# Optimization experiments

Measured on AMD Instinct MI355X. Metric: run time of the kernel, lower is better.

The kernel has to match this reference:

```python
import jax, jax.numpy as jnp
import numpy as np

B, D, H = 4096, 1024, 1024

def _glorot(key, shape):
    fan_in, fan_out = shape
    limit = np.sqrt(6.0 / (fan_in + fan_out))
    return jax.random.uniform(key, shape, jnp.float32, -limit, limit)

def setup_inputs() -> dict:
    key = jax.random.key(0)
    ks = jax.random.split(key, 12)
    inp = {
        'inputs': jax.random.normal(ks[0], (B, D), jnp.float32),
        'h_prev': jax.random.normal(ks[1], (B, H), jnp.float32),
        'c_prev': jax.random.normal(ks[2], (B, H), jnp.float32),
    }
    names = ['f', 'i', 'c', 'o']
    for j, n in enumerate(names):
        inp['W_' + n] = _glorot(ks[3 + 2 * j], (D, H))
        inp['U_' + n] = _glorot(ks[4 + 2 * j], (H, H))
        inp['b_' + n] = jnp.zeros((H,), jnp.float32)
    return inp

def reference(inputs, h_prev, c_prev, W_f, U_f, b_f, W_i, U_i, b_i, W_c, U_c, b_c, W_o, U_o, b_o):
    f_t = jax.nn.sigmoid(inputs @ W_f + h_prev @ U_f + b_f)
    i_t = jax.nn.sigmoid(inputs @ W_i + h_prev @ U_i + b_i)
    c_tilde = jnp.tanh(inputs @ W_c + h_prev @ U_c + b_c)
    c_next = f_t * c_prev + i_t * c_tilde
    o_t = jax.nn.sigmoid(inputs @ W_o + h_prev @ U_o + b_o)
    h_next = o_t * jnp.tanh(c_next)
    return (h_next, c_next)
```

## Files before the change

kernel.cpp:

```cpp
#include <hip/hip_runtime.h>


typedef __attribute__((ext_vector_type(8))) short bfrag8;

__device__ __forceinline__ unsigned int f2bf(float f) {
  unsigned int u = __builtin_bit_cast(unsigned int, f);
  unsigned int r = (u + 0x7fffu + ((u >> 16) & 1u)) >> 16;
  return r & 0xffffu;
}

__global__ __launch_bounds__(256) void prep_x(const float* __restrict__ inputs,
                                              const float* __restrict__ h_prev,
                                              unsigned short* __restrict__ X) {
  int idx = blockIdx.x * 256 + threadIdx.x;
  int b  = idx >> 8;
  int k8 = (idx & 255) * 8;
  const float* src = (k8 < 1024) ? (inputs + (size_t)b * 1024 + k8)
                                 : (h_prev + (size_t)b * 1024 + (k8 - 1024));
  float4 v0 = ((const float4*)src)[0];
  float4 v1 = ((const float4*)src)[1];
  uint4 o;
  o.x = f2bf(v0.x) | (f2bf(v0.y) << 16);
  o.y = f2bf(v0.z) | (f2bf(v0.w) << 16);
  o.z = f2bf(v1.x) | (f2bf(v1.y) << 16);
  o.w = f2bf(v1.z) | (f2bf(v1.w) << 16);
  *(uint4*)(X + (size_t)b * 2048 + k8) = o;
}

__global__ __launch_bounds__(256) void prep_w(
    const float* __restrict__ s0, const float* __restrict__ s1,
    const float* __restrict__ s2, const float* __restrict__ s3,
    const float* __restrict__ s4, const float* __restrict__ s5,
    const float* __restrict__ s6, const float* __restrict__ s7,
    unsigned short* __restrict__ Wct) {
  int blk = blockIdx.x;
  int m = blk >> 8;
  const float* src = (m == 0) ? s0 : (m == 1) ? s1 : (m == 2) ? s2 : (m == 3) ? s3
                   : (m == 4) ? s4 : (m == 5) ? s5 : (m == 6) ? s6 : s7;
  int g = m >> 1, half = m & 1;
  unsigned short* dst = Wct + (size_t)g * 1024 * 2048 + (size_t)half * 1024;
  int t = blk & 255;
  int k0 = (t >> 4) * 64;
  int h0 = (t & 15) * 64;
  __shared__ float lt[64][68];
  int tid = threadIdx.x;
  #pragma unroll
  for (int it = 0; it < 4; ++it) {
    int r  = (tid >> 4) + it * 16;
    int c4 = (tid & 15) * 4;
    float4 v = *(const float4*)(src + (size_t)(k0 + r) * 1024 + h0 + c4);
    lt[r][c4 + 0] = v.x; lt[r][c4 + 1] = v.y; lt[r][c4 + 2] = v.z; lt[r][c4 + 3] = v.w;
  }
  __syncthreads();
  #pragma unroll
  for (int it = 0; it < 4; ++it) {
    int hh  = (tid >> 4) + it * 16;
    int kk4 = (tid & 15) * 4;
    uint2 o;
    o.x = f2bf(lt[kk4 + 0][hh]) | (f2bf(lt[kk4 + 1][hh]) << 16);
    o.y = f2bf(lt[kk4 + 2][hh]) | (f2bf(lt[kk4 + 3][hh]) << 16);
    *(uint2*)(dst + (size_t)(h0 + hh) * 2048 + k0 + kk4) = o;
  }
}


#define FENCE() asm volatile("" ::: "memory")
#define BARRIER() do { FENCE(); __builtin_amdgcn_s_barrier(); FENCE(); } while (0)
#define VMCNT(n) asm volatile("s_waitcnt vmcnt(" #n ")" ::: "memory")
#define LGKM(n) asm volatile("s_waitcnt lgkmcnt(" #n ")" ::: "memory")
#define GLOAD16(gp, lp) __builtin_amdgcn_global_load_lds( \
    (const __attribute__((address_space(1))) unsigned int*)(gp), \
    (__attribute__((address_space(3))) unsigned int*)(lp), 16, 0, 0)
#define DSR(dst, addr, off) asm volatile("ds_read_b128 %0, %1 offset:%c2" \
    : "=v"(dst) : "v"(addr), "n"(off))

#define AC "a0","a1","a2","a3","a4","a5","a6","a7","a8","a9","a10","a11","a12","a13","a14","a15", \
 "a16","a17","a18","a19","a20","a21","a22","a23","a24","a25","a26","a27","a28","a29","a30","a31", \
 "a32","a33","a34","a35","a36","a37","a38","a39","a40","a41","a42","a43","a44","a45","a46","a47", \
 "a48","a49","a50","a51","a52","a53","a54","a55","a56","a57","a58","a59","a60","a61","a62","a63", \
 "a64","a65","a66","a67","a68","a69","a70","a71","a72","a73","a74","a75","a76","a77","a78","a79", \
 "a80","a81","a82","a83","a84","a85","a86","a87","a88","a89","a90","a91","a92","a93","a94","a95", \
 "a96","a97","a98","a99","a100","a101","a102","a103","a104","a105","a106","a107","a108","a109","a110","a111", \
 "a112","a113","a114","a115","a116","a117","a118","a119","a120","a121","a122","a123","a124","a125","a126","a127"

#define WZ(n) "v_accvgpr_write_b32 a" #n ", 0\n\t"
#define AINIT() asm volatile( \
 WZ(0)WZ(1)WZ(2)WZ(3)WZ(4)WZ(5)WZ(6)WZ(7)WZ(8)WZ(9)WZ(10)WZ(11)WZ(12)WZ(13)WZ(14)WZ(15) \
 WZ(16)WZ(17)WZ(18)WZ(19)WZ(20)WZ(21)WZ(22)WZ(23)WZ(24)WZ(25)WZ(26)WZ(27)WZ(28)WZ(29)WZ(30)WZ(31) \
 WZ(32)WZ(33)WZ(34)WZ(35)WZ(36)WZ(37)WZ(38)WZ(39)WZ(40)WZ(41)WZ(42)WZ(43)WZ(44)WZ(45)WZ(46)WZ(47) \
 WZ(48)WZ(49)WZ(50)WZ(51)WZ(52)WZ(53)WZ(54)WZ(55)WZ(56)WZ(57)WZ(58)WZ(59)WZ(60)WZ(61)WZ(62)WZ(63) \
 WZ(64)WZ(65)WZ(66)WZ(67)WZ(68)WZ(69)WZ(70)WZ(71)WZ(72)WZ(73)WZ(74)WZ(75)WZ(76)WZ(77)WZ(78)WZ(79) \
 WZ(80)WZ(81)WZ(82)WZ(83)WZ(84)WZ(85)WZ(86)WZ(87)WZ(88)WZ(89)WZ(90)WZ(91)WZ(92)WZ(93)WZ(94)WZ(95) \
 WZ(96)WZ(97)WZ(98)WZ(99)WZ(100)WZ(101)WZ(102)WZ(103)WZ(104)WZ(105)WZ(106)WZ(107)WZ(108)WZ(109)WZ(110)WZ(111) \
 WZ(112)WZ(113)WZ(114)WZ(115)WZ(116)WZ(117)WZ(118)WZ(119)WZ(120)WZ(121)WZ(122)WZ(123)WZ(124)WZ(125)WZ(126)WZ(127) \
 ::: AC)

#define MFMA_ONE(BR, AF, BF) asm volatile( \
    "v_mfma_f32_16x16x32_bf16 a[" BR "], %0, %1, a[" BR "]" \
    :: "v"(AF), "v"(BF) : AC)

#define CLUSTER16(A4, B4, R00,R01,R02,R03, R10,R11,R12,R13, R20,R21,R22,R23, R30,R31,R32,R33) do { \
  __builtin_amdgcn_s_setprio(1); \
  MFMA_ONE(R00, (A4)[0], (B4)[0]); MFMA_ONE(R01, (A4)[1], (B4)[0]); \
  MFMA_ONE(R02, (A4)[2], (B4)[0]); MFMA_ONE(R03, (A4)[3], (B4)[0]); \
  MFMA_ONE(R10, (A4)[0], (B4)[1]); MFMA_ONE(R11, (A4)[1], (B4)[1]); \
  MFMA_ONE(R12, (A4)[2], (B4)[1]); MFMA_ONE(R13, (A4)[3], (B4)[1]); \
  MFMA_ONE(R20, (A4)[0], (B4)[2]); MFMA_ONE(R21, (A4)[1], (B4)[2]); \
  MFMA_ONE(R22, (A4)[2], (B4)[2]); MFMA_ONE(R23, (A4)[3], (B4)[2]); \
  MFMA_ONE(R30, (A4)[0], (B4)[3]); MFMA_ONE(R31, (A4)[1], (B4)[3]); \
  MFMA_ONE(R32, (A4)[2], (B4)[3]); MFMA_ONE(R33, (A4)[3], (B4)[3]); \
  __builtin_amdgcn_s_setprio(0); \
} while (0)

#define CL_MH0(A4, B4) CLUSTER16(A4, B4, \
  "0:3","4:7","8:11","12:15", "32:35","36:39","40:43","44:47", \
  "64:67","68:71","72:75","76:79", "96:99","100:103","104:107","108:111")
#define CL_MH1(A4, B4) CLUSTER16(A4, B4, \
  "16:19","20:23","24:27","28:31", "48:51","52:55","56:59","60:63", \
  "80:83","84:87","88:91","92:95", "112:115","116:119","120:123","124:127")

#define READ_A4(arr, BUF, MH, ABASE) do { \
  DSR(arr[0], ABASE, (BUF)*32768 + (MH)*8192 + 0);    \
  DSR(arr[1], ABASE, (BUF)*32768 + (MH)*8192 + 2048); \
  DSR(arr[2], ABASE, (BUF)*32768 + (MH)*8192 + 4096); \
  DSR(arr[3], ABASE, (BUF)*32768 + (MH)*8192 + 6144); \
} while (0)

#define READ_B4N(arr, BUF, BBASE) do { \
  DSR(arr[0], BBASE, (BUF)*32768 + 0);    \
  DSR(arr[1], BBASE, (BUF)*32768 + 2048); \
  DSR(arr[2], BBASE, (BUF)*32768 + 4096); \
  DSR(arr[3], BBASE, (BUF)*32768 + 6144); \
} while (0)

#define STAGE_A(BUF, H, kt) do { int _kb = ((kt) < 32 ? (kt) : 31) * 64; \
  GLOAD16(pA0 + (size_t)(H) * 262144 + _kb, smem + (BUF)*32768 + (H)*16384 + stbase); \
  GLOAD16(pA1 + (size_t)(H) * 262144 + _kb, smem + (BUF)*32768 + (H)*16384 + stbase + 1024); \
} while (0)

#define STAGE_B(BUF, kt) do { int _kb = ((kt) < 32 ? (kt) : 31) * 64; \
  GLOAD16(pB00 + _kb, smem + 65536 + (BUF)*32768 + stbase); \
  GLOAD16(pB01 + _kb, smem + 65536 + (BUF)*32768 + stbase + 1024); \
  GLOAD16(pB10 + _kb, smem + 65536 + (BUF)*32768 + 16384 + stbase); \
  GLOAD16(pB11 + _kb, smem + 65536 + (BUF)*32768 + 16384 + stbase + 1024); \
} while (0)

#define ARD(X, RS) asm volatile("v_accvgpr_read_b32 %0, " RS : "=v"(X))

#define EPI_M(Mi, F0,F1,F2,F3, I0,I1,I2,I3, C0,C1,C2,C3, O0,O1,O2,O3) do { \
  float pf[4], pi[4], pc[4], po[4]; \
  ARD(pf[0],F0); ARD(pf[1],F1); ARD(pf[2],F2); ARD(pf[3],F3); \
  ARD(pi[0],I0); ARD(pi[1],I1); ARD(pi[2],I2); ARD(pi[3],I3); \
  ARD(pc[0],C0); ARD(pc[1],C1); ARD(pc[2],C2); ARD(pc[3],C3); \
  ARD(po[0],O0); ARD(po[1],O1); ARD(po[2],O2); ARD(po[3],O3); \
  _Pragma("unroll") for (int j = 0; j < 4; ++j) { \
    const int b = rbw + (Mi) * 16 + q * 4 + j; \
    float xf = pf[j] + Bgf, xi = pi[j] + Bgi, xc = pc[j] + Bgc, xo = po[j] + Bgo; \
    float fg = 1.f / (1.f + __expf(-xf)); \
    float ig = 1.f / (1.f + __expf(-xi)); \
    float ct = 2.f / (1.f + __expf(-2.f * xc)) - 1.f; \
    float og = 1.f / (1.f + __expf(-xo)); \
    float cn = fg * c_prev[(size_t)b * 1024 + hcol] + ig * ct; \
    float hn = og * (2.f / (1.f + __expf(-2.f * cn)) - 1.f); \
    out[(size_t)b * 1024 + hcol] = hn; \
    out[(size_t)4194304 + (size_t)b * 1024 + hcol] = cn; \
  } \
} while (0)

__global__ __launch_bounds__(512, 2) void lstm_gemm(
    const unsigned short* __restrict__ X, const unsigned short* __restrict__ Wct,
    const float* __restrict__ c_prev,
    const float* __restrict__ bfv, const float* __restrict__ biv,
    const float* __restrict__ bcv, const float* __restrict__ bov,
    float* __restrict__ out) {
  extern __shared__ __align__(16) char smem[];
  const int tid = threadIdx.x;
  const int lane = tid & 63, w = tid >> 6;
  const int u = lane & 15, q = (lane >> 4) & 3;
  const int wm = w >> 2, wn = w & 3;

  const int bid = blockIdx.x;
  const int swz = (bid & 7) * 32 + (bid >> 3);
  const int h0 = (swz & 15) * 64;
  const int row0 = (swz >> 4) * 256;

  const unsigned lds0 = (unsigned)(size_t)((__attribute__((address_space(3))) char*)smem);

  const int sw0 = (q ^ (u & 7)) << 4;
  const int sw1 = ((q + 4) ^ (u & 7)) << 4;
  const unsigned aA0 = lds0 + wm * 16384 + u * 128 + sw0;
  const unsigned aA1 = lds0 + wm * 16384 + u * 128 + sw1;
  const unsigned aB0 = lds0 + 65536 + (wn * 64 + u) * 128 + sw0;
  const unsigned aB1 = lds0 + 65536 + (wn * 64 + u) * 128 + sw1;

  const int stbase = w * 2048 + lane * 16;
  const int rA0 = w * 16 + (lane >> 3), rA1 = rA0 + 8;
  const int ssA = (lane & 7) ^ (rA0 & 7);
  const unsigned short* pA0 = X + (size_t)(row0 + rA0) * 2048 + ssA * 8;
  const unsigned short* pA1 = X + (size_t)(row0 + rA1) * 2048 + ssA * 8;
  auto wrow = [&](int C) { return (((C >> 4) & 3) << 10) + h0 + ((C >> 6) << 4) + (C & 15); };
  const unsigned short* pB00 = Wct + (size_t)wrow(rA0) * 2048 + ssA * 8;
  const unsigned short* pB01 = Wct + (size_t)wrow(rA1) * 2048 + ssA * 8;
  const unsigned short* pB10 = Wct + (size_t)wrow(128 + rA0) * 2048 + ssA * 8;
  const unsigned short* pB11 = Wct + (size_t)wrow(128 + rA1) * 2048 + ssA * 8;

  AINIT();

  bfrag8 Ab0[4], Ab1[4], Bb0[4], Bb1[4];

  STAGE_A(0, 0, 0); STAGE_A(0, 1, 0);
  STAGE_B(0, 0);
  STAGE_B(1, 1);
  VMCNT(4);
  BARRIER();
  READ_A4(Ab0, 0, 0, aA0);
  READ_B4N(Bb0, 0, aB0);

  #pragma unroll 1
  for (int t = 0; t < 16; ++t) {
    const int kt1 = 2 * t + 1, kt2 = 2 * t + 2, kt3 = 2 * t + 3;
    READ_A4(Ab1, 0, 1, aA0);
    STAGE_A(1, 0, kt1); STAGE_A(1, 1, kt1);
    BARRIER(); LGKM(4);
    CL_MH0(Ab0, Bb0);
    READ_A4(Ab0, 0, 0, aA1);
    READ_B4N(Bb1, 0, aB1);
    BARRIER(); LGKM(8);
    CL_MH1(Ab1, Bb0);
    READ_A4(Ab1, 0, 1, aA1);
    VMCNT(0);
    BARRIER(); LGKM(4);
    CL_MH0(Ab0, Bb1);
    READ_A4(Ab0, 1, 0, aA0);
    READ_B4N(Bb0, 1, aB0);
    STAGE_B(0, kt2);
    BARRIER(); LGKM(8);
    CL_MH1(Ab1, Bb1);
    READ_A4(Ab1, 1, 1, aA0);
    STAGE_A(0, 0, kt2); STAGE_A(0, 1, kt2);
    BARRIER(); LGKM(4);
    CL_MH0(Ab0, Bb0);
    READ_A4(Ab0, 1, 0, aA1);
    READ_B4N(Bb1, 1, aB1);
    BARRIER(); LGKM(8);
    CL_MH1(Ab1, Bb0);
    READ_A4(Ab1, 1, 1, aA1);
    VMCNT(0);
    BARRIER(); LGKM(4);
    CL_MH0(Ab0, Bb1);
    READ_A4(Ab0, 0, 0, aA0);
    READ_B4N(Bb0, 0, aB0);
    STAGE_B(1, kt3);
    BARRIER(); LGKM(8);
    CL_MH1(Ab1, Bb1);
  }
  VMCNT(0); LGKM(0);
  asm volatile("s_nop 7\n\ts_nop 7");

  const int hcol = h0 + wn * 16 + u;
  const float Bgf = bfv[hcol], Bgi = biv[hcol], Bgc = bcv[hcol], Bgo = bov[hcol];
  const int rbw = row0 + wm * 128;
  EPI_M(0, "a0","a1","a2","a3",     "a32","a33","a34","a35",
           "a64","a65","a66","a67", "a96","a97","a98","a99");
  EPI_M(1, "a4","a5","a6","a7",     "a36","a37","a38","a39",
           "a68","a69","a70","a71", "a100","a101","a102","a103");
  EPI_M(2, "a8","a9","a10","a11",   "a40","a41","a42","a43",
           "a72","a73","a74","a75", "a104","a105","a106","a107");
  EPI_M(3, "a12","a13","a14","a15", "a44","a45","a46","a47",
           "a76","a77","a78","a79", "a108","a109","a110","a111");
  EPI_M(4, "a16","a17","a18","a19", "a48","a49","a50","a51",
           "a80","a81","a82","a83", "a112","a113","a114","a115");
  EPI_M(5, "a20","a21","a22","a23", "a52","a53","a54","a55",
           "a84","a85","a86","a87", "a116","a117","a118","a119");
  EPI_M(6, "a24","a25","a26","a27", "a56","a57","a58","a59",
           "a88","a89","a90","a91", "a120","a121","a122","a123");
  EPI_M(7, "a28","a29","a30","a31", "a60","a61","a62","a63",
           "a92","a93","a94","a95", "a124","a125","a126","a127");
}

extern "C" void kernel_launch(void* const* d_in, const int* in_sizes, int n_in,
                              void* d_out, int out_size, void* d_ws, size_t ws_size,
                              hipStream_t stream) {
  const float* inputs = (const float*)d_in[0];
  const float* h_prev = (const float*)d_in[1];
  const float* c_prev = (const float*)d_in[2];
  const float* Wf = (const float*)d_in[3];
  const float* Uf = (const float*)d_in[4];
  const float* bf = (const float*)d_in[5];
  const float* Wi = (const float*)d_in[6];
  const float* Ui = (const float*)d_in[7];
  const float* bi = (const float*)d_in[8];
  const float* Wc = (const float*)d_in[9];
  const float* Uc = (const float*)d_in[10];
  const float* bc = (const float*)d_in[11];
  const float* Wo = (const float*)d_in[12];
  const float* Uo = (const float*)d_in[13];
  const float* bo = (const float*)d_in[14];
  float* out = (float*)d_out;

  unsigned short* X   = (unsigned short*)d_ws;
  unsigned short* Wct = X + (size_t)4096 * 2048;

  (void)hipFuncSetAttribute(reinterpret_cast<const void*>(lstm_gemm),
                            hipFuncAttributeMaxDynamicSharedMemorySize, 131072);

  prep_x<<<4096, 256, 0, stream>>>(inputs, h_prev, X);
  prep_w<<<2048, 256, 0, stream>>>(Wf, Uf, Wi, Ui, Wc, Uc, Wo, Uo, Wct);
  lstm_gemm<<<256, 512, 131072, stream>>>(X, Wct, c_prev, bf, bi, bc, bo, out);
}
```

Before: 87.58 us.

## Shrink GEMM tile to 256x128 with K=32 steps for higher occupancy

The GEMM block tile drops from 256 rows by 256 gate-columns to 256 rows by 128 columns, with K-steps of 32 instead of 64. Each wave now holds 64 accumulators instead of 128, LDS use falls from 128 KiB to 48 KiB, and launch bounds ask for four blocks per CU. The intricate half-tile interleaved software pipeline is replaced by a simple double-buffered loop that waits on all loads and barriers twice per iteration. The aim is more blocks (512) and better occupancy to fill all CUs, at the cost of lower data reuse per block and less fine-grained overlap of loads with MFMA.

```diff
diff --git a/kernel.cpp b/kernel.cpp
--- a/kernel.cpp
+++ b/kernel.cpp
@@ -66,8 +66,8 @@
 
 #define FENCE() asm volatile("" ::: "memory")
 #define BARRIER() do { FENCE(); __builtin_amdgcn_s_barrier(); FENCE(); } while (0)
-#define VMCNT(n) asm volatile("s_waitcnt vmcnt(" #n ")" ::: "memory")
-#define LGKM(n) asm volatile("s_waitcnt lgkmcnt(" #n ")" ::: "memory")
+#define VMCNT0() asm volatile("s_waitcnt vmcnt(0)" ::: "memory")
+#define LGKM0() asm volatile("s_waitcnt lgkmcnt(0)" ::: "memory")
 #define GLOAD16(gp, lp) __builtin_amdgcn_global_load_lds( \
     (const __attribute__((address_space(1))) unsigned int*)(gp), \
     (__attribute__((address_space(3))) unsigned int*)(lp), 16, 0, 0)
@@ -77,11 +77,7 @@
 #define AC "a0","a1","a2","a3","a4","a5","a6","a7","a8","a9","a10","a11","a12","a13","a14","a15", \
  "a16","a17","a18","a19","a20","a21","a22","a23","a24","a25","a26","a27","a28","a29","a30","a31", \
  "a32","a33","a34","a35","a36","a37","a38","a39","a40","a41","a42","a43","a44","a45","a46","a47", \
- "a48","a49","a50","a51","a52","a53","a54","a55","a56","a57","a58","a59","a60","a61","a62","a63", \
- "a64","a65","a66","a67","a68","a69","a70","a71","a72","a73","a74","a75","a76","a77","a78","a79", \
- "a80","a81","a82","a83","a84","a85","a86","a87","a88","a89","a90","a91","a92","a93","a94","a95", \
- "a96","a97","a98","a99","a100","a101","a102","a103","a104","a105","a106","a107","a108","a109","a110","a111", \
- "a112","a113","a114","a115","a116","a117","a118","a119","a120","a121","a122","a123","a124","a125","a126","a127"
+ "a48","a49","a50","a51","a52","a53","a54","a55","a56","a57","a58","a59","a60","a61","a62","a63"
 
 #define WZ(n) "v_accvgpr_write_b32 a" #n ", 0\n\t"
 #define AINIT() asm volatile( \
@@ -89,60 +85,43 @@
  WZ(16)WZ(17)WZ(18)WZ(19)WZ(20)WZ(21)WZ(22)WZ(23)WZ(24)WZ(25)WZ(26)WZ(27)WZ(28)WZ(29)WZ(30)WZ(31) \
  WZ(32)WZ(33)WZ(34)WZ(35)WZ(36)WZ(37)WZ(38)WZ(39)WZ(40)WZ(41)WZ(42)WZ(43)WZ(44)WZ(45)WZ(46)WZ(47) \
  WZ(48)WZ(49)WZ(50)WZ(51)WZ(52)WZ(53)WZ(54)WZ(55)WZ(56)WZ(57)WZ(58)WZ(59)WZ(60)WZ(61)WZ(62)WZ(63) \
- WZ(64)WZ(65)WZ(66)WZ(67)WZ(68)WZ(69)WZ(70)WZ(71)WZ(72)WZ(73)WZ(74)WZ(75)WZ(76)WZ(77)WZ(78)WZ(79) \
- WZ(80)WZ(81)WZ(82)WZ(83)WZ(84)WZ(85)WZ(86)WZ(87)WZ(88)WZ(89)WZ(90)WZ(91)WZ(92)WZ(93)WZ(94)WZ(95) \
- WZ(96)WZ(97)WZ(98)WZ(99)WZ(100)WZ(101)WZ(102)WZ(103)WZ(104)WZ(105)WZ(106)WZ(107)WZ(108)WZ(109)WZ(110)WZ(111) \
- WZ(112)WZ(113)WZ(114)WZ(115)WZ(116)WZ(117)WZ(118)WZ(119)WZ(120)WZ(121)WZ(122)WZ(123)WZ(124)WZ(125)WZ(126)WZ(127) \
  ::: AC)
 
 #define MFMA_ONE(BR, AF, BF) asm volatile( \
     "v_mfma_f32_16x16x32_bf16 a[" BR "], %0, %1, a[" BR "]" \
     :: "v"(AF), "v"(BF) : AC)
 
-#define CLUSTER16(A4, B4, R00,R01,R02,R03, R10,R11,R12,R13, R20,R21,R22,R23, R30,R31,R32,R33) do { \
+#define CL16() do { \
   __builtin_amdgcn_s_setprio(1); \
-  MFMA_ONE(R00, (A4)[0], (B4)[0]); MFMA_ONE(R01, (A4)[1], (B4)[0]); \
-  MFMA_ONE(R02, (A4)[2], (B4)[0]); MFMA_ONE(R03, (A4)[3], (B4)[0]); \
-  MFMA_ONE(R10, (A4)[0], (B4)[1]); MFMA_ONE(R11, (A4)[1], (B4)[1]); \
-  MFMA_ONE(R12, (A4)[2], (B4)[1]); MFMA_ONE(R13, (A4)[3], (B4)[1]); \
-  MFMA_ONE(R20, (A4)[0], (B4)[2]); MFMA_ONE(R21, (A4)[1], (B4)[2]); \
-  MFMA_ONE(R22, (A4)[2], (B4)[2]); MFMA_ONE(R23, (A4)[3], (B4)[2]); \
-  MFMA_ONE(R30, (A4)[0], (B4)[3]); MFMA_ONE(R31, (A4)[1], (B4)[3]); \
-  MFMA_ONE(R32, (A4)[2], (B4)[3]); MFMA_ONE(R33, (A4)[3], (B4)[3]); \
+  MFMA_ONE("0:3",   Af[0], Bf[0]); MFMA_ONE("4:7",   Af[1], Bf[0]); \
+  MFMA_ONE("8:11",  Af[2], Bf[0]); MFMA_ONE("12:15", Af[3], Bf[0]); \
+  MFMA_ONE("16:19", Af[0], Bf[1]); MFMA_ONE("20:23", Af[1], Bf[1]); \
+  MFMA_ONE("24:27", Af[2], Bf[1]); MFMA_ONE("28:31", Af[3], Bf[1]); \
+  MFMA_ONE("32:35", Af[0], Bf[2]); MFMA_ONE("36:39", Af[1], Bf[2]); \
+  MFMA_ONE("40:43", Af[2], Bf[2]); MFMA_ONE("44:47", Af[3], Bf[2]); \
+  MFMA_ONE("48:51", Af[0], Bf[3]); MFMA_ONE("52:55", Af[1], Bf[3]); \
+  MFMA_ONE("56:59", Af[2], Bf[3]); MFMA_ONE("60:63", Af[3], Bf[3]); \
   __builtin_amdgcn_s_setprio(0); \
 } while (0)
 
-#define CL_MH0(A4, B4) CLUSTER16(A4, B4, \
-  "0:3","4:7","8:11","12:15", "32:35","36:39","40:43","44:47", \
-  "64:67","68:71","72:75","76:79", "96:99","100:103","104:107","108:111")
-#define CL_MH1(A4, B4) CLUSTER16(A4, B4, \
-  "16:19","20:23","24:27","28:31", "48:51","52:55","56:59","60:63", \
-  "80:83","84:87","88:91","92:95", "112:115","116:119","120:123","124:127")
-
-#define READ_A4(arr, BUF, MH, ABASE) do { \
-  DSR(arr[0], ABASE, (BUF)*32768 + (MH)*8192 + 0);    \
-  DSR(arr[1], ABASE, (BUF)*32768 + (MH)*8192 + 2048); \
-  DSR(arr[2], ABASE, (BUF)*32768 + (MH)*8192 + 4096); \
-  DSR(arr[3], ABASE, (BUF)*32768 + (MH)*8192 + 6144); \
-} while (0)
-
-#define READ_B4N(arr, BUF, BBASE) do { \
-  DSR(arr[0], BBASE, (BUF)*32768 + 0);    \
-  DSR(arr[1], BBASE, (BUF)*32768 + 2048); \
-  DSR(arr[2], BBASE, (BUF)*32768 + 4096); \
-  DSR(arr[3], BBASE, (BUF)*32768 + 6144); \
-} while (0)
-
-#define STAGE_A(BUF, H, kt) do { int _kb = ((kt) < 32 ? (kt) : 31) * 64; \
-  GLOAD16(pA0 + (size_t)(H) * 262144 + _kb, smem + (BUF)*32768 + (H)*16384 + stbase); \
-  GLOAD16(pA1 + (size_t)(H) * 262144 + _kb, smem + (BUF)*32768 + (H)*16384 + stbase + 1024); \
-} while (0)
-
-#define STAGE_B(BUF, kt) do { int _kb = ((kt) < 32 ? (kt) : 31) * 64; \
-  GLOAD16(pB00 + _kb, smem + 65536 + (BUF)*32768 + stbase); \
-  GLOAD16(pB01 + _kb, smem + 65536 + (BUF)*32768 + stbase + 1024); \
-  GLOAD16(pB10 + _kb, smem + 65536 + (BUF)*32768 + 16384 + stbase); \
-  GLOAD16(pB11 + _kb, smem + 65536 + (BUF)*32768 + 16384 + stbase + 1024); \
+#define READ_A(BUF) do { \
+  DSR(Af[0], aAb, (BUF)*16384 + 0);    \
+  DSR(Af[1], aAb, (BUF)*16384 + 1024); \
+  DSR(Af[2], aAb, (BUF)*16384 + 2048); \
+  DSR(Af[3], aAb, (BUF)*16384 + 3072); \
+} while (0)
+
+#define READ_B(BUF) do { \
+  DSR(Bf[0], aBb, (BUF)*8192 + 0);    \
+  DSR(Bf[1], aBb, (BUF)*8192 + 1024); \
+  DSR(Bf[2], aBb, (BUF)*8192 + 2048); \
+  DSR(Bf[3], aBb, (BUF)*8192 + 3072); \
+} while (0)
+
+#define STAGE(BUF, kt) do { int _kb = ((kt) < 64 ? (kt) : 63) * 32; \
+  GLOAD16(pA0 + _kb, smem + (BUF)*16384 + stb); \
+  GLOAD16(pA1 + _kb, smem + (BUF)*16384 + 8192 + stb); \
+  GLOAD16(pBs + _kb, smem + 32768 + (BUF)*8192 + stb); \
 } while (0)
 
 #define ARD(X, RS) asm volatile("v_accvgpr_read_b32 %0, " RS : "=v"(X))
@@ -167,7 +146,7 @@
   } \
 } while (0)
 
-__global__ __launch_bounds__(512, 2) void lstm_gemm(
+__global__ __launch_bounds__(512, 4) void lstm_gemm(
     const unsigned short* __restrict__ X, const unsigned short* __restrict__ Wct,
     const float* __restrict__ c_prev,
     const float* __restrict__ bfv, const float* __restrict__ biv,
@@ -177,105 +156,64 @@
   const int tid = threadIdx.x;
   const int lane = tid & 63, w = tid >> 6;
   const int u = lane & 15, q = (lane >> 4) & 3;
-  const int wm = w >> 2, wn = w & 3;
+  const int wm = w >> 1, wn = w & 1;
 
   const int bid = blockIdx.x;
-  const int swz = (bid & 7) * 32 + (bid >> 3);
-  const int h0 = (swz & 15) * 64;
-  const int row0 = (swz >> 4) * 256;
+  const int swz = (bid & 7) * 64 + (bid >> 3);
+  const int row0 = (swz >> 5) * 256;
+  const int h0 = (swz & 31) * 32;
 
   const unsigned lds0 = (unsigned)(size_t)((__attribute__((address_space(3))) char*)smem);
 
-  const int sw0 = (q ^ (u & 7)) << 4;
-  const int sw1 = ((q + 4) ^ (u & 7)) << 4;
-  const unsigned aA0 = lds0 + wm * 16384 + u * 128 + sw0;
-  const unsigned aA1 = lds0 + wm * 16384 + u * 128 + sw1;
-  const unsigned aB0 = lds0 + 65536 + (wn * 64 + u) * 128 + sw0;
-  const unsigned aB1 = lds0 + 65536 + (wn * 64 + u) * 128 + sw1;
-
-  const int stbase = w * 2048 + lane * 16;
-  const int rA0 = w * 16 + (lane >> 3), rA1 = rA0 + 8;
-  const int ssA = (lane & 7) ^ (rA0 & 7);
-  const unsigned short* pA0 = X + (size_t)(row0 + rA0) * 2048 + ssA * 8;
-  const unsigned short* pA1 = X + (size_t)(row0 + rA1) * 2048 + ssA * 8;
-  auto wrow = [&](int C) { return (((C >> 4) & 3) << 10) + h0 + ((C >> 6) << 4) + (C & 15); };
-  const unsigned short* pB00 = Wct + (size_t)wrow(rA0) * 2048 + ssA * 8;
-  const unsigned short* pB01 = Wct + (size_t)wrow(rA1) * 2048 + ssA * 8;
-  const unsigned short* pB10 = Wct + (size_t)wrow(128 + rA0) * 2048 + ssA * 8;
-  const unsigned short* pB11 = Wct + (size_t)wrow(128 + rA1) * 2048 + ssA * 8;
+  const int fsw = (q ^ ((u >> 1) & 3)) << 4;
+  const unsigned aAb = lds0 + (wm * 64 + u) * 64 + fsw;
+  const unsigned aBb = lds0 + 32768 + (wn * 64 + u) * 64 + fsw;
+
+  const int stb = tid * 16;
+  const int srow = tid >> 2;
+  const int sg = (tid & 3) ^ ((tid >> 3) & 3);
+  const unsigned short* pA0 = X + (size_t)(row0 + srow) * 2048 + sg * 8;
+  const unsigned short* pA1 = X + (size_t)(row0 + 128 + srow) * 2048 + sg * 8;
+  const int bg = (srow >> 4) & 3;
+  const int wr = bg * 1024 + h0 + (srow >> 6) * 16 + (srow & 15);
+  const unsigned short* pBs = Wct + (size_t)wr * 2048 + sg * 8;
 
   AINIT();
-
-  bfrag8 Ab0[4], Ab1[4], Bb0[4], Bb1[4];
-
-  STAGE_A(0, 0, 0); STAGE_A(0, 1, 0);
-  STAGE_B(0, 0);
-  STAGE_B(1, 1);
-  VMCNT(4);
+  bfrag8 Af[4], Bf[4];
+
+  STAGE(0, 0);
+  VMCNT0();
   BARRIER();
-  READ_A4(Ab0, 0, 0, aA0);
-  READ_B4N(Bb0, 0, aB0);
 
   #pragma unroll 1
-  for (int t = 0; t < 16; ++t) {
-    const int kt1 = 2 * t + 1, kt2 = 2 * t + 2, kt3 = 2 * t + 3;
-    READ_A4(Ab1, 0, 1, aA0);
-    STAGE_A(1, 0, kt1); STAGE_A(1, 1, kt1);
-    BARRIER(); LGKM(4);
-    CL_MH0(Ab0, Bb0);
-    READ_A4(Ab0, 0, 0, aA1);
-    READ_B4N(Bb1, 0, aB1);
-    BARRIER(); LGKM(8);
-    CL_MH1(Ab1, Bb0);
-    READ_A4(Ab1, 0, 1, aA1);
-    VMCNT(0);
-    BARRIER(); LGKM(4);
-    CL_MH0(Ab0, Bb1);
-    READ_A4(Ab0, 1, 0, aA0);
-    READ_B4N(Bb0, 1, aB0);
-    STAGE_B(0, kt2);
-    BARRIER(); LGKM(8);
-    CL_MH1(Ab1, Bb1);
-    READ_A4(Ab1, 1, 1, aA0);
-    STAGE_A(0, 0, kt2); STAGE_A(0, 1, kt2);
-    BARRIER(); LGKM(4);
-    CL_MH0(Ab0, Bb0);
-    READ_A4(Ab0, 1, 0, aA1);
-    READ_B4N(Bb1, 1, aB1);
-    BARRIER(); LGKM(8);
-    CL_MH1(Ab1, Bb0);
-    READ_A4(Ab1, 1, 1, aA1);
-    VMCNT(0);
-    BARRIER(); LGKM(4);
-    CL_MH0(Ab0, Bb1);
-    READ_A4(Ab0, 0, 0, aA0);
-    READ_B4N(Bb0, 0, aB0);
-    STAGE_B(1, kt3);
-    BARRIER(); LGKM(8);
-    CL_MH1(Ab1, Bb1);
+  for (int tt = 0; tt < 32; ++tt) {
+    const int t1 = 2 * tt + 1, t2 = 2 * tt + 2;
+    READ_A(0); READ_B(0);
+    STAGE(1, t1);
+    LGKM0();
+    CL16();
+    VMCNT0();
+    BARRIER();
+    READ_A(1); READ_B(1);
+    STAGE(0, t2);
+    LGKM0();
+    CL16();
+    VMCNT0();
+    BARRIER();
   }
-  VMCNT(0); LGKM(0);
   asm volatile("s_nop 7\n\ts_nop 7");
 
   const int hcol = h0 + wn * 16 + u;
   const float Bgf = bfv[hcol], Bgi = biv[hcol], Bgc = bcv[hcol], Bgo = bov[hcol];
-  const int rbw = row0 + wm * 128;
-  EPI_M(0, "a0","a1","a2","a3",     "a32","a33","a34","a35",
-           "a64","a65","a66","a67", "a96","a97","a98","a99");
-  EPI_M(1, "a4","a5","a6","a7",     "a36","a37","a38","a39",
-           "a68","a69","a70","a71", "a100","a101","a102","a103");
-  EPI_M(2, "a8","a9","a10","a11",   "a40","a41","a42","a43",
-           "a72","a73","a74","a75", "a104","a105","a106","a107");
-  EPI_M(3, "a12","a13","a14","a15", "a44","a45","a46","a47",
-           "a76","a77","a78","a79", "a108","a109","a110","a111");
-  EPI_M(4, "a16","a17","a18","a19", "a48","a49","a50","a51",
-           "a80","a81","a82","a83", "a112","a113","a114","a115");
-  EPI_M(5, "a20","a21","a22","a23", "a52","a53","a54","a55",
-           "a84","a85","a86","a87", "a116","a117","a118","a119");
-  EPI_M(6, "a24","a25","a26","a27", "a56","a57","a58","a59",
-           "a88","a89","a90","a91", "a120","a121","a122","a123");
-  EPI_M(7, "a28","a29","a30","a31", "a60","a61","a62","a63",
-           "a92","a93","a94","a95", "a124","a125","a126","a127");
+  const int rbw = row0 + wm * 64;
+  EPI_M(0, "a0","a1","a2","a3",     "a16","a17","a18","a19",
+           "a32","a33","a34","a35", "a48","a49","a50","a51");
+  EPI_M(1, "a4","a5","a6","a7",     "a20","a21","a22","a23",
+           "a36","a37","a38","a39", "a52","a53","a54","a55");
+  EPI_M(2, "a8","a9","a10","a11",   "a24","a25","a26","a27",
+           "a40","a41","a42","a43", "a56","a57","a58","a59");
+  EPI_M(3, "a12","a13","a14","a15", "a28","a29","a30","a31",
+           "a44","a45","a46","a47", "a60","a61","a62","a63");
 }
 
 extern "C" void kernel_launch(void* const* d_in, const int* in_sizes, int n_in,
@@ -302,9 +240,9 @@
   unsigned short* Wct = X + (size_t)4096 * 2048;
 
   (void)hipFuncSetAttribute(reinterpret_cast<const void*>(lstm_gemm),
-                            hipFuncAttributeMaxDynamicSharedMemorySize, 131072);
+                            hipFuncAttributeMaxDynamicSharedMemorySize, 49152);
 
   prep_x<<<4096, 256, 0, stream>>>(inputs, h_prev, X);
   prep_w<<<2048, 256, 0, stream>>>(Wf, Uf, Wi, Ui, Wc, Uc, Wo, Uo, Wct);
-  lstm_gemm<<<256, 512, 131072, stream>>>(X, Wct, c_prev, bf, bi, bc, bo, out);
-}
+  lstm_gemm<<<512, 512, 49152, stream>>>(X, Wct, c_prev, bf, bi, bc, bo, out);
+}
```

Result: slower. 101.1 us (+15.5%).
